# Kernel tuning notes

Hardware: AMD Instinct MI355X
Metric: run time of the kernel (lower is better)

Reference implementation:

```python
import jax, jax.numpy as jnp
import numpy as np

B = 8192
DIM = 64
NUM_USERS = 100000
NUM_ITEMS = 100000
GAMMA = 1.0


def setup_inputs() -> dict:
    key = jax.random.key(0)
    k1, k2, k3, k4, k5 = jax.random.split(key, 5)
    return {
        "user_id": jax.random.randint(k1, (B,), 0, NUM_USERS, dtype=jnp.int64)
        if jax.config.jax_enable_x64 else jax.random.randint(k1, (B,), 0, NUM_USERS, dtype=jnp.int32),
        "pos_id": jax.random.randint(k2, (B,), 0, NUM_ITEMS, dtype=jnp.int32),
        "neg_id": jax.random.randint(k3, (B,), 0, NUM_ITEMS, dtype=jnp.int32),
        "user_table": jax.random.normal(k4, (NUM_USERS, DIM), dtype=jnp.float32) * 0.01,
        "item_table": jax.random.normal(k5, (NUM_ITEMS, DIM), dtype=jnp.float32) * 0.01,
    }


def _normalize(x):
    return x / jnp.linalg.norm(x, axis=-1, keepdims=True)


def _alignment(x, y):
    # F.normalize then mean squared L2 distance over the batch
    xn, yn = _normalize(x), _normalize(y)
    return jnp.mean(jnp.sum((xn - yn) ** 2, axis=1))


def _uniformity(x):
    # log mean_{i<j} exp(-2 * ||xi - xj||^2) on normalized rows.
    # For unit vectors: ||xi - xj||^2 = 2 - 2 <xi, xj>. Use the full Gram
    # matrix; diagonal contributes exp(0)=1 per row, removed in closed form.
    xn = _normalize(x)
    n = xn.shape[0]
    sim = xn @ xn.T                      # [B, B]
    e = jnp.exp(-2.0 * (2.0 - 2.0 * sim))  # [B, B]
    pair_sum = (jnp.sum(e) - n) * 0.5    # sum over i<j
    n_pairs = n * (n - 1) // 2
    return jnp.log(pair_sum / n_pairs)


def reference(user_id, pos_id, neg_id, user_table, item_table):
    user_e = user_table[user_id]   # [B, DIM]
    pos_e = item_table[pos_id]     # [B, DIM]
    align = _alignment(user_e, pos_e)
    uniform = (_uniformity(user_e) + _uniformity(pos_e)) * 0.5
    return align + GAMMA * uniform
```

## Files before the change

kernel.cpp:

```cpp
#include <hip/hip_runtime.h>
#include <hip/hip_bf16.h>
#include <math.h>

#define NROWS 8192
#define DIM 64
#define NTILE 64
#define NPAIRS 2080

typedef __bf16 bf16x8 __attribute__((ext_vector_type(8)));
typedef float f32x4 __attribute__((ext_vector_type(4)));


__global__ __launch_bounds__(256) void gather_norm_kernel(
    const int* __restrict__ user_id, const int* __restrict__ pos_id,
    const float* __restrict__ user_table, const float* __restrict__ item_table,
    float* __restrict__ part_align,
    __hip_bfloat16* __restrict__ Xu, __hip_bfloat16* __restrict__ Xp)
{
    const int lane = threadIdx.x & 63;
    const int w    = threadIdx.x >> 6;
    const int row  = blockIdx.x * 4 + w;

    const float u = user_table[(long)user_id[row] * DIM + lane];
    const float p = item_table[(long)pos_id[row] * DIM + lane];

    float su = u * u, sp = p * p;
    #pragma unroll
    for (int m = 32; m >= 1; m >>= 1) {
        su += __shfl_xor(su, m, 64);
        sp += __shfl_xor(sp, m, 64);
    }
    const float un = u * rsqrtf(su);
    const float pn = p * rsqrtf(sp);

    Xu[row * DIM + lane] = __float2bfloat16(un);
    Xp[row * DIM + lane] = __float2bfloat16(pn);

    const float d = un - pn;
    float dd = d * d;
    #pragma unroll
    for (int m = 32; m >= 1; m >>= 1) dd += __shfl_xor(dd, m, 64);

    __shared__ float red[4];
    if (lane == 0) red[w] = dd;
    __syncthreads();
    if (threadIdx.x == 0)
        part_align[blockIdx.x] = red[0] + red[1] + red[2] + red[3];
}

__global__ __launch_bounds__(256) void gram_exp_kernel(
    const __hip_bfloat16* __restrict__ Xu, const __hip_bfloat16* __restrict__ Xp,
    float* __restrict__ part_gram)
{
    const int t = blockIdx.x;
    const int z = blockIdx.y;
    const __hip_bfloat16* __restrict__ X = (z == 0) ? Xu : Xp;

    int i = (int)((sqrtf(8.0f * (float)t + 1.0f) - 1.0f) * 0.5f);
    while (i * (i + 1) / 2 > t) --i;
    while ((i + 1) * (i + 2) / 2 <= t) ++i;
    const int j = t - i * (i + 1) / 2;
    const int bi = j, bj = i;

    const int tid  = threadIdx.x;
    const int lane = tid & 63;
    const int w    = tid >> 6;
    const int wr   = w >> 1, wc = w & 1;
    const int r    = lane & 15;
    const int quad = lane >> 4;

    __shared__ __align__(16) char lds[2 * 16384];

    {
        const char* srcA = (const char*)(X + (size_t)bi * 128 * DIM);
        const char* srcB = (const char*)(X + (size_t)bj * 128 * DIM);
        const int l16 = lane * 16;
        #pragma unroll
        for (int k = 0; k < 4; ++k) {
            const int x  = w * 4096 + k * 1024 + l16;
            const int sx = x ^ (((x >> 7) & 7) << 4);
            *reinterpret_cast<bf16x8*>(lds + sx) =
                *reinterpret_cast<const bf16x8*>(srcA + x);
            *reinterpret_cast<bf16x8*>(lds + 16384 + sx) =
                *reinterpret_cast<const bf16x8*>(srcB + x);
        }
    }
    __syncthreads();

    bf16x8 a[4][2], b[4][2];
    #pragma unroll
    for (int tt = 0; tt < 4; ++tt) {
        const int rowA = wr * 64 + tt * 16 + r;
        const int cA   = (quad * 16) ^ ((rowA & 7) << 4);
        a[tt][0] = *reinterpret_cast<const bf16x8*>(lds + rowA * 128 + cA);
        a[tt][1] = *reinterpret_cast<const bf16x8*>(lds + rowA * 128 + (cA ^ 64));
        const int rowB = wc * 64 + tt * 16 + r;
        const int cB   = (quad * 16) ^ ((rowB & 7) << 4);
        b[tt][0] = *reinterpret_cast<const bf16x8*>(lds + 16384 + rowB * 128 + cB);
        b[tt][1] = *reinterpret_cast<const bf16x8*>(lds + 16384 + rowB * 128 + (cB ^ 64));
    }

    f32x4 acc[4][4];
    #pragma unroll
    for (int mt = 0; mt < 4; ++mt)
        #pragma unroll
        for (int nt = 0; nt < 4; ++nt) {
            f32x4 c = {0.f, 0.f, 0.f, 0.f};
            c = __builtin_amdgcn_mfma_f32_16x16x32_bf16(a[mt][0], b[nt][0], c, 0, 0, 0);
            c = __builtin_amdgcn_mfma_f32_16x16x32_bf16(a[mt][1], b[nt][1], c, 0, 0, 0);
            acc[mt][nt] = c;
        }

    const float C4 = 5.770780163555851f;
    float s0 = 0.f, s1 = 0.f, s2 = 0.f, s3 = 0.f;
    #pragma unroll
    for (int mt = 0; mt < 4; ++mt)
        #pragma unroll
        for (int nt = 0; nt < 4; ++nt) {
            s0 += __builtin_amdgcn_exp2f(fmaf(C4, acc[mt][nt][0], -C4));
            s1 += __builtin_amdgcn_exp2f(fmaf(C4, acc[mt][nt][1], -C4));
            s2 += __builtin_amdgcn_exp2f(fmaf(C4, acc[mt][nt][2], -C4));
            s3 += __builtin_amdgcn_exp2f(fmaf(C4, acc[mt][nt][3], -C4));
        }
    float s = (s0 + s1) + (s2 + s3);

    #pragma unroll
    for (int m = 32; m >= 1; m >>= 1) s += __shfl_xor(s, m, 64);

    __shared__ float red[4];
    if (lane == 0) red[w] = s;
    __syncthreads();
    if (tid == 0) {
        const float wgt = (bi == bj) ? 1.f : 2.f;
        part_gram[z * NPAIRS + t] = wgt * (red[0] + red[1] + red[2] + red[3]);
    }
}

__global__ __launch_bounds__(256) void finalize_kernel(
    const float* __restrict__ part_align, const float* __restrict__ part_gram,
    float* __restrict__ out)
{
    float a = 0.f, su = 0.f, sp = 0.f;
    for (int k = threadIdx.x; k < 2048; k += 256)   a  += part_align[k];
    for (int k = threadIdx.x; k < NPAIRS; k += 256) su += part_gram[k];
    for (int k = threadIdx.x; k < NPAIRS; k += 256) sp += part_gram[NPAIRS + k];

    #pragma unroll
    for (int m = 32; m >= 1; m >>= 1) {
        a  += __shfl_xor(a, m, 64);
        su += __shfl_xor(su, m, 64);
        sp += __shfl_xor(sp, m, 64);
    }
    __shared__ float ra[4], ru[4], rp[4];
    const int w = threadIdx.x >> 6, lane = threadIdx.x & 63;
    if (lane == 0) { ra[w] = a; ru[w] = su; rp[w] = sp; }
    __syncthreads();
    if (threadIdx.x == 0) {
        const float A  = ra[0] + ra[1] + ra[2] + ra[3];
        const float SU = ru[0] + ru[1] + ru[2] + ru[3];
        const float SP = rp[0] + rp[1] + rp[2] + rp[3];
        const float n = 8192.f;
        const float npairs = 8192.f * 8191.f * 0.5f;
        const float pu = (SU - n) * 0.5f;
        const float pp = (SP - n) * 0.5f;
        out[0] = A / n + 0.5f * (logf(pu / npairs) + logf(pp / npairs));
    }
}

extern "C" void kernel_launch(void* const* d_in, const int* in_sizes, int n_in,
                              void* d_out, int out_size, void* d_ws, size_t ws_size,
                              hipStream_t stream)
{
    const int*   user_id    = (const int*)d_in[0];
    const int*   pos_id     = (const int*)d_in[1];
    const float* user_table = (const float*)d_in[3];
    const float* item_table = (const float*)d_in[4];
    float* out = (float*)d_out;

    float* part_align = (float*)d_ws;
    float* part_gram  = (float*)((char*)d_ws + 8192);
    __hip_bfloat16* Xu = (__hip_bfloat16*)((char*)d_ws + 32768);
    __hip_bfloat16* Xp = Xu + (size_t)NROWS * DIM;

    gather_norm_kernel<<<NROWS / 4, 256, 0, stream>>>(
        user_id, pos_id, user_table, item_table, part_align, Xu, Xp);

    gram_exp_kernel<<<dim3(NPAIRS, 2), 256, 0, stream>>>(Xu, Xp, part_gram);

    finalize_kernel<<<1, 256, 0, stream>>>(part_align, part_gram, out);
}
```

Before: 116.6 us.

## Enlarge Gram tiles to 256x256 and interleave MFMA with exp per row strip

After: 113.2 us. 1.03x faster.

```diff
diff --git a/kernel.cpp b/kernel.cpp
--- a/kernel.cpp
+++ b/kernel.cpp
@@ -4,8 +4,8 @@
 
 #define NROWS 8192
 #define DIM 64
-#define NTILE 64
-#define NPAIRS 2080
+#define NTILE 32
+#define NPAIRS 528
 
 typedef __bf16 bf16x8 __attribute__((ext_vector_type(8)));
 typedef float f32x4 __attribute__((ext_vector_type(4)));
@@ -69,59 +69,57 @@
     const int r    = lane & 15;
     const int quad = lane >> 4;
 
-    __shared__ __align__(16) char lds[2 * 16384];
+    __shared__ __align__(16) char lds[2 * 32768];
 
     {
-        const char* srcA = (const char*)(X + (size_t)bi * 128 * DIM);
-        const char* srcB = (const char*)(X + (size_t)bj * 128 * DIM);
-        const int l16 = lane * 16;
+        const char* srcA = (const char*)(X + (size_t)bi * 256 * DIM);
+        const char* srcB = (const char*)(X + (size_t)bj * 256 * DIM);
         #pragma unroll
-        for (int k = 0; k < 4; ++k) {
-            const int x  = w * 4096 + k * 1024 + l16;
+        for (int k = 0; k < 8; ++k) {
+            const int x  = (k * 256 + tid) * 16;
             const int sx = x ^ (((x >> 7) & 7) << 4);
             *reinterpret_cast<bf16x8*>(lds + sx) =
                 *reinterpret_cast<const bf16x8*>(srcA + x);
-            *reinterpret_cast<bf16x8*>(lds + 16384 + sx) =
+            *reinterpret_cast<bf16x8*>(lds + 32768 + sx) =
                 *reinterpret_cast<const bf16x8*>(srcB + x);
         }
     }
     __syncthreads();
 
-    bf16x8 a[4][2], b[4][2];
+    bf16x8 b[8][2];
     #pragma unroll
-    for (int tt = 0; tt < 4; ++tt) {
-        const int rowA = wr * 64 + tt * 16 + r;
-        const int cA   = (quad * 16) ^ ((rowA & 7) << 4);
-        a[tt][0] = *reinterpret_cast<const bf16x8*>(lds + rowA * 128 + cA);
-        a[tt][1] = *reinterpret_cast<const bf16x8*>(lds + rowA * 128 + (cA ^ 64));
-        const int rowB = wc * 64 + tt * 16 + r;
+    for (int tt = 0; tt < 8; ++tt) {
+        const int rowB = wc * 128 + tt * 16 + r;
         const int cB   = (quad * 16) ^ ((rowB & 7) << 4);
-        b[tt][0] = *reinterpret_cast<const bf16x8*>(lds + 16384 + rowB * 128 + cB);
-        b[tt][1] = *reinterpret_cast<const bf16x8*>(lds + 16384 + rowB * 128 + (cB ^ 64));
+        b[tt][0] = *reinterpret_cast<const bf16x8*>(lds + 32768 + rowB * 128 + cB);
+        b[tt][1] = *reinterpret_cast<const bf16x8*>(lds + 32768 + rowB * 128 + (cB ^ 64));
     }
-
-    f32x4 acc[4][4];
-    #pragma unroll
-    for (int mt = 0; mt < 4; ++mt)
-        #pragma unroll
-        for (int nt = 0; nt < 4; ++nt) {
-            f32x4 c = {0.f, 0.f, 0.f, 0.f};
-            c = __builtin_amdgcn_mfma_f32_16x16x32_bf16(a[mt][0], b[nt][0], c, 0, 0, 0);
-            c = __builtin_amdgcn_mfma_f32_16x16x32_bf16(a[mt][1], b[nt][1], c, 0, 0, 0);
-            acc[mt][nt] = c;
-        }
 
     const float C4 = 5.770780163555851f;
     float s0 = 0.f, s1 = 0.f, s2 = 0.f, s3 = 0.f;
     #pragma unroll
-    for (int mt = 0; mt < 4; ++mt)
+    for (int mt = 0; mt < 8; ++mt) {
+        const int rowA = wr * 128 + mt * 16 + r;
+        const int cA   = (quad * 16) ^ ((rowA & 7) << 4);
+        const bf16x8 a0 = *reinterpret_cast<const bf16x8*>(lds + rowA * 128 + cA);
+        const bf16x8 a1 = *reinterpret_cast<const bf16x8*>(lds + rowA * 128 + (cA ^ 64));
+
+        f32x4 c[8];
         #pragma unroll
-        for (int nt = 0; nt < 4; ++nt) {
-            s0 += __builtin_amdgcn_exp2f(fmaf(C4, acc[mt][nt][0], -C4));
-            s1 += __builtin_amdgcn_exp2f(fmaf(C4, acc[mt][nt][1], -C4));
-            s2 += __builtin_amdgcn_exp2f(fmaf(C4, acc[mt][nt][2], -C4));
-            s3 += __builtin_amdgcn_exp2f(fmaf(C4, acc[mt][nt][3], -C4));
+        for (int nt = 0; nt < 8; ++nt) {
+            f32x4 cc = {0.f, 0.f, 0.f, 0.f};
+            cc = __builtin_amdgcn_mfma_f32_16x16x32_bf16(a0, b[nt][0], cc, 0, 0, 0);
+            cc = __builtin_amdgcn_mfma_f32_16x16x32_bf16(a1, b[nt][1], cc, 0, 0, 0);
+            c[nt] = cc;
         }
+        #pragma unroll
+        for (int nt = 0; nt < 8; ++nt) {
+            s0 += __builtin_amdgcn_exp2f(fmaf(C4, c[nt][0], -C4));
+            s1 += __builtin_amdgcn_exp2f(fmaf(C4, c[nt][1], -C4));
+            s2 += __builtin_amdgcn_exp2f(fmaf(C4, c[nt][2], -C4));
+            s3 += __builtin_amdgcn_exp2f(fmaf(C4, c[nt][3], -C4));
+        }
+    }
     float s = (s0 + s1) + (s2 + s3);
 
     #pragma unroll
```
